# Kernel tuning notes

Measured on AMD Instinct MI355X. Metric: run time of the kernel, lower is better.

## Reference

```python
import jax, jax.numpy as jnp
import numpy as np

CH = 256
B, H, W = 8, 128, 128
CQK = CH // 8


def _conv1x1(x, w, b):
    # x: [B,C,H,W], w: [O,C], b: [O]
    return jnp.einsum('bchw,oc->bohw', x, w) + b[None, :, None, None]


def setup_inputs() -> dict:
    key = jax.random.key(0)
    ks = jax.random.split(key, 8)
    sq = 1.0 / np.sqrt(CH)
    return {
        'x': jax.random.normal(ks[0], (B, CH, H, W), dtype=jnp.float32),
        'Wq': jax.random.normal(ks[1], (CQK, CH), dtype=jnp.float32) * sq,
        'bq': jax.random.normal(ks[2], (CQK,), dtype=jnp.float32) * 0.01,
        'Wk': jax.random.normal(ks[3], (CQK, CH), dtype=jnp.float32) * sq,
        'bk': jax.random.normal(ks[4], (CQK,), dtype=jnp.float32) * 0.01,
        'Wv': jax.random.normal(ks[5], (CH, CH), dtype=jnp.float32) * sq,
        'bv': jax.random.normal(ks[6], (CH,), dtype=jnp.float32) * 0.01,
        'gamma': jax.random.normal(ks[7], (1,), dtype=jnp.float32) * 0.1,
        'recurrence': 2,
    }


def reference(x, Wq, bq, Wk, bk, Wv, bv, gamma, recurrence):
    q = _conv1x1(x, Wq, bq)   # [B, C//8, H, W]
    k = _conv1x1(x, Wk, bk)   # [B, C//8, H, W]
    v = _conv1x1(x, Wv, bv)   # [B, C, H, W]
    if recurrence % 2 == 1:
        # attention along W, independently per (b, h); no mask
        energy = jnp.einsum('bchi,bchj->bhij', q, k)      # [B,H,W,W]
        att = jax.nn.softmax(energy, axis=-1)
        out = jnp.einsum('bchj,bhij->bchi', v, att)       # [B,C,H,W]
    else:
        # attention along H, independently per (b, w); diagonal masked -inf
        energy = jnp.einsum('bciw,bcjw->bwij', q, k)      # [B,W,H,H]
        h = energy.shape[-1]
        diag = jnp.eye(h, dtype=bool)[None, None]
        energy = jnp.where(diag, -jnp.inf, energy)
        att = jax.nn.softmax(energy, axis=-1)             # [B,W,H,H]
        out = jnp.einsum('bcjw,bwij->bciw', v, att)       # [B,C,H,W]
    return gamma[0] * out + x
```

## Files before the change

### kernel.cpp

```cpp
#include <hip/hip_runtime.h>
#include <hip/hip_bf16.h>

#define B_   8
#define CH_  256
#define CQK_ 32
#define H_   128
#define W_   128

typedef __attribute__((ext_vector_type(8))) short s16x8;
typedef __attribute__((ext_vector_type(4))) float f32x4;
typedef __attribute__((ext_vector_type(4))) unsigned short u16x4;

__device__ __forceinline__ unsigned short f2b(float f) {
  __hip_bfloat16 h = __float2bfloat16(f);
  return *(unsigned short*)&h;
}
__device__ __forceinline__ float b2f(unsigned short u) {
  return __uint_as_float(((unsigned)u) << 16);
}


__global__ void kw_pack(const float* __restrict__ Wq, const float* __restrict__ Wk,
                        const float* __restrict__ Wv, unsigned short* __restrict__ wqk,
                        unsigned short* __restrict__ wv) {
  int idx = blockIdx.x * 256 + threadIdx.x;
  if (idx < 64 * 256) {
    int qc = idx >> 8, c = idx & 255;
    wqk[idx] = f2b(qc < 32 ? Wq[qc * 256 + c] : Wk[(qc - 32) * 256 + c]);
  } else {
    int i2 = idx - 64 * 256;
    wv[i2] = f2b(Wv[i2]);
  }
}

__global__ __launch_bounds__(256) void k0_xpose(const float* __restrict__ x,
                                                unsigned short* __restrict__ xt) {
  __shared__ unsigned short st[256 * 137];
  const int t = threadIdx.x;
  const int b = blockIdx.x >> 7;
  const int h = blockIdx.x & 127;
  const float* xin = x + ((size_t)b * 256 * 128 + h) * 128;
  const int w = t & 127, chalf = t >> 7;
#pragma unroll 8
  for (int it = 0; it < 128; ++it) {
    int c = it * 2 + chalf;
    st[c * 137 + w] = f2b(xin[(size_t)c * 16384 + w]);
  }
  __syncthreads();
  unsigned short* xo = xt + ((size_t)b * 128 * 128 + h) * 256;
  const int cl = t & 127, whalf = t >> 7;
#pragma unroll 8
  for (int it = 0; it < 64; ++it) {
    int wr = it * 2 + whalf;
    unsigned v = (unsigned)st[(2 * cl) * 137 + wr] |
                 ((unsigned)st[(2 * cl + 1) * 137 + wr] << 16);
    *(unsigned*)&xo[(size_t)wr * 32768 + 2 * cl] = v;
  }
}

__global__ __launch_bounds__(256, 2) void k0b_xpose(const unsigned short* __restrict__ xt,
                                                    unsigned short* __restrict__ xt2) {
  __shared__ unsigned short st[128 * 264];
  const int t = threadIdx.x;
  const size_t colbase = (size_t)blockIdx.x * 32768;
#pragma unroll
  for (int it = 0; it < 16; ++it) {
    int ch = it * 256 + t;
    int row = ch >> 5, off = (ch & 31) * 8;
    *(uint4*)&st[row * 264 + off] = *(const uint4*)&xt[colbase + ch * 8];
  }
  __syncthreads();
  const int hpl = t & 3, cq = t >> 2;
#pragma unroll 8
  for (int it = 0; it < 64; ++it) {
    const int itc = it & 3, ith = it >> 2;
    const int c = itc * 64 + cq;
    const int hp = ith * 4 + hpl;
    unsigned v = (unsigned)st[(2 * hp) * 264 + c] |
                 ((unsigned)st[(2 * hp + 1) * 264 + c] << 16);
    *(unsigned*)&xt2[colbase + (size_t)c * 128 + hp * 2] = v;
  }
}

struct SmemY {
  unsigned short qt[128 * 40];
  unsigned short kt[128 * 40];
  unsigned short att[128 * 136];
};

__global__ __launch_bounds__(256, 2)
void k1y(const unsigned short* __restrict__ xt, const unsigned short* __restrict__ xt2,
         const unsigned short* __restrict__ wqk, const float* __restrict__ bq,
         const float* __restrict__ bk, unsigned short* __restrict__ y) {
  __shared__ SmemY sm;
  const int t = threadIdx.x;
  const int wvid = t >> 6;
  const int lane = t & 63;
  const int l15 = lane & 15;
  const int quad = lane >> 4;
  const int b = blockIdx.x >> 7;
  const int w = blockIdx.x & 127;
  const size_t colbase = ((size_t)b * 128 + w) * 32768;

  {
    const int qc0 = wvid * 16;
    f32x4 acc[8];
#pragma unroll
    for (int nt = 0; nt < 8; ++nt) acc[nt] = {0.f, 0.f, 0.f, 0.f};
    const unsigned short* arow = wqk + (qc0 + l15) * 256 + quad * 8;
    const unsigned short* bcol = xt + colbase + (size_t)l15 * 256 + quad * 8;
#pragma unroll
    for (int kk = 0; kk < 8; ++kk) {
      s16x8 a = *(const s16x8*)(arow + kk * 32);
#pragma unroll
      for (int nt = 0; nt < 8; ++nt) {
        s16x8 bb = *(const s16x8*)(bcol + nt * 16 * 256 + kk * 32);
        acc[nt] = __builtin_amdgcn_mfma_f32_16x16x32_bf16(a, bb, acc[nt], 0, 0, 0);
      }
    }
    const float* bp = (wvid < 2) ? bq : bk;
    const int qcl = qc0 & 16;
    float bias[4];
#pragma unroll
    for (int r = 0; r < 4; ++r) bias[r] = bp[qcl + quad * 4 + r];
    unsigned short* dst = (wvid < 2) ? sm.qt : sm.kt;
#pragma unroll
    for (int nt = 0; nt < 8; ++nt) {
      int h = nt * 16 + l15;
      u16x4 pk;
#pragma unroll
      for (int r = 0; r < 4; ++r) pk[r] = f2b(acc[nt][r] + bias[r]);
      *(u16x4*)&dst[h * 40 + qcl + quad * 4] = pk;
    }
  }
  __syncthreads();

  {
    const int i0 = wvid * 32;
    s16x8 aQ[2];
#pragma unroll
    for (int mt = 0; mt < 2; ++mt)
      aQ[mt] = *(const s16x8*)&sm.qt[(i0 + mt * 16 + l15) * 40 + quad * 8];
    f32x4 eacc[2][8];
#pragma unroll
    for (int mt = 0; mt < 2; ++mt)
#pragma unroll
      for (int nt = 0; nt < 8; ++nt) eacc[mt][nt] = {0.f, 0.f, 0.f, 0.f};
#pragma unroll
    for (int nt = 0; nt < 8; ++nt) {
      s16x8 bK = *(const s16x8*)&sm.kt[(nt * 16 + l15) * 40 + quad * 8];
      eacc[0][nt] = __builtin_amdgcn_mfma_f32_16x16x32_bf16(aQ[0], bK, eacc[0][nt], 0, 0, 0);
      eacc[1][nt] = __builtin_amdgcn_mfma_f32_16x16x32_bf16(aQ[1], bK, eacc[1][nt], 0, 0, 0);
    }
#pragma unroll
    for (int mt = 0; mt < 2; ++mt)
#pragma unroll
      for (int nt = 0; nt < 8; ++nt) {
        const int j = nt * 16 + l15;
#pragma unroll
        for (int r = 0; r < 4; ++r)
          if (j == i0 + mt * 16 + quad * 4 + r) eacc[mt][nt][r] = -__builtin_inff();
      }
#pragma unroll
    for (int mt = 0; mt < 2; ++mt)
#pragma unroll
      for (int r = 0; r < 4; ++r) {
        float mx = -__builtin_inff();
#pragma unroll
        for (int nt = 0; nt < 8; ++nt) mx = fmaxf(mx, eacc[mt][nt][r]);
        mx = fmaxf(mx, __shfl_xor(mx, 1));
        mx = fmaxf(mx, __shfl_xor(mx, 2));
        mx = fmaxf(mx, __shfl_xor(mx, 4));
        mx = fmaxf(mx, __shfl_xor(mx, 8));
        float s = 0.f;
#pragma unroll
        for (int nt = 0; nt < 8; ++nt) {
          float p = __expf(eacc[mt][nt][r] - mx);
          eacc[mt][nt][r] = p;
          s += p;
        }
        s += __shfl_xor(s, 1);
        s += __shfl_xor(s, 2);
        s += __shfl_xor(s, 4);
        s += __shfl_xor(s, 8);
        const float inv = 1.0f / s;
        const int i = i0 + mt * 16 + quad * 4 + r;
#pragma unroll
        for (int nt = 0; nt < 8; ++nt)
          sm.att[i * 136 + nt * 16 + l15] = f2b(eacc[mt][nt][r] * inv);
      }
  }
  __syncthreads();

  f32x4 yacc[8][4];
#pragma unroll
  for (int mt = 0; mt < 8; ++mt)
#pragma unroll
    for (int nt = 0; nt < 4; ++nt) yacc[mt][nt] = {0.f, 0.f, 0.f, 0.f};
  {
    const int c0 = wvid * 64;
#pragma unroll
    for (int kj = 0; kj < 4; ++kj) {
      s16x8 aP[8];
#pragma unroll
      for (int mt = 0; mt < 8; ++mt)
        aP[mt] = *(const s16x8*)&sm.att[(mt * 16 + l15) * 136 + kj * 32 + quad * 8];
#pragma unroll
      for (int nt = 0; nt < 4; ++nt) {
        s16x8 bX = *(const s16x8*)&xt2[colbase + (size_t)(c0 + nt * 16 + l15) * 128 +
                                        kj * 32 + quad * 8];
#pragma unroll
        for (int mt = 0; mt < 8; ++mt)
          yacc[mt][nt] = __builtin_amdgcn_mfma_f32_16x16x32_bf16(aP[mt], bX, yacc[mt][nt], 0, 0, 0);
      }
    }
  }
#pragma unroll 1
  for (int h2 = 0; h2 < 2; ++h2) {
    __syncthreads();
    if ((wvid >> 1) == h2) {
      const int clb = (wvid & 1) * 64;
#pragma unroll
      for (int mt = 0; mt < 8; ++mt)
#pragma unroll
        for (int nt = 0; nt < 4; ++nt) {
          const int cl = clb + nt * 16 + l15;
#pragma unroll
          for (int r = 0; r < 4; ++r)
            sm.att[(mt * 16 + quad * 4 + r) * 136 + cl] = f2b(yacc[mt][nt][r]);
        }
    }
    __syncthreads();
#pragma unroll
    for (int it = 0; it < 8; ++it) {
      int g = it * 256 + t;
      int i = g >> 4, cc = (g & 15) * 8;
      *(uint4*)&y[((size_t)(b * 128 + i) * 128 + w) * 256 + h2 * 128 + cc] =
          *(const uint4*)&sm.att[i * 136 + cc];
    }
  }
}

__global__ __launch_bounds__(256, 2)
void k2g(const unsigned short* __restrict__ y, const unsigned short* __restrict__ wv,
         const float* __restrict__ bv, const float* __restrict__ gamma,
         const float* __restrict__ x, float* __restrict__ out) {
  const int t = threadIdx.x;
  const int wvid = t >> 6;
  const int lane = t & 63;
  const int l15 = lane & 15;
  const int quad = lane >> 4;
  const int b = blockIdx.x >> 7;
  const int h = blockIdx.x & 127;
  const int m0 = wvid * 64;
  f32x4 acc[4][8];
#pragma unroll
  for (int mt = 0; mt < 4; ++mt)
#pragma unroll
    for (int nt = 0; nt < 8; ++nt) acc[mt][nt] = {0.f, 0.f, 0.f, 0.f};
  const unsigned short* arow = wv + (m0 + l15) * 256 + quad * 8;
  const unsigned short* brow = y + ((size_t)(b * 128 + h) * 128 + l15) * 256 + quad * 8;
#pragma unroll
  for (int kk = 0; kk < 8; ++kk) {
    s16x8 a[4];
#pragma unroll
    for (int mt = 0; mt < 4; ++mt)
      a[mt] = *(const s16x8*)(arow + mt * 16 * 256 + kk * 32);
#pragma unroll
    for (int nt = 0; nt < 8; ++nt) {
      s16x8 bb = *(const s16x8*)(brow + nt * 16 * 256 + kk * 32);
#pragma unroll
      for (int mt = 0; mt < 4; ++mt)
        acc[mt][nt] = __builtin_amdgcn_mfma_f32_16x16x32_bf16(a[mt], bb, acc[mt][nt], 0, 0, 0);
    }
  }
  const float g = gamma[0];
#pragma unroll
  for (int mt = 0; mt < 4; ++mt)
#pragma unroll
    for (int r = 0; r < 4; ++r) {
      const int co = m0 + mt * 16 + quad * 4 + r;
      const float bvv = bv[co];
      const size_t base = ((size_t)(b * 256 + co) * 128 + h) * 128;
#pragma unroll
      for (int nt = 0; nt < 8; ++nt) {
        const int wc = nt * 16 + l15;
        out[base + wc] = g * (acc[mt][nt][r] + bvv) + x[base + wc];
      }
    }
}


struct SmemK1 {
  __hip_bfloat16 x[CH_][H_];
  float att[H_][130];
  union {
    struct { __hip_bfloat16 q[CQK_][H_]; __hip_bfloat16 k[CQK_][H_]; } qk;
    float vchunk[32][130];
  } s;
};

__device__ __forceinline__ void load_bf16x16(const __hip_bfloat16* p, float* f) {
  const uint4* p4 = (const uint4*)p;
  uint4 a = p4[0], b = p4[1];
  unsigned uu[8] = {a.x, a.y, a.z, a.w, b.x, b.y, b.z, b.w};
#pragma unroll
  for (int m = 0; m < 8; ++m) {
    f[2 * m] = __uint_as_float(uu[m] << 16);
    f[2 * m + 1] = __uint_as_float(uu[m] & 0xffff0000u);
  }
}

__global__ __launch_bounds__(256, 1)
void k1_attn(const float* __restrict__ x, const float* __restrict__ Wq,
             const float* __restrict__ bq, const float* __restrict__ Wk,
             const float* __restrict__ bk, const float* __restrict__ Wv,
             const float* __restrict__ bv, float* __restrict__ o_t) {
  __shared__ SmemK1 sm;
  const int t = threadIdx.x;
  const int b = blockIdx.x >> 7;
  const int w = blockIdx.x & 127;
  {
    const float* xb = x + (size_t)b * CH_ * H_ * W_ + w;
    const int h = t & 127;
    const int c0 = (t >> 7) * 128;
#pragma unroll 8
    for (int r = 0; r < 128; ++r) {
      const int c = c0 + r;
      sm.x[c][h] = __float2bfloat16(xb[(size_t)(c * H_ + h) * W_]);
    }
  }
  __syncthreads();
  {
    const int qc = t >> 3;
    const int i0 = (t & 7) << 4;
    float qa[16], ka[16];
    const float bqv = bq[qc], bkv = bk[qc];
#pragma unroll
    for (int u = 0; u < 16; ++u) { qa[u] = bqv; ka[u] = bkv; }
    const float* wqr = Wq + qc * CH_;
    const float* wkr = Wk + qc * CH_;
    for (int c = 0; c < CH_; c += 4) {
      const float4 wq4 = *(const float4*)(wqr + c);
      const float4 wk4 = *(const float4*)(wkr + c);
      const float wqs[4] = {wq4.x, wq4.y, wq4.z, wq4.w};
      const float wks[4] = {wk4.x, wk4.y, wk4.z, wk4.w};
#pragma unroll
      for (int cc = 0; cc < 4; ++cc) {
        float xf[16];
        load_bf16x16(&sm.x[c + cc][i0], xf);
#pragma unroll
        for (int u = 0; u < 16; ++u) {
          qa[u] += wqs[cc] * xf[u];
          ka[u] += wks[cc] * xf[u];
        }
      }
    }
#pragma unroll
    for (int u = 0; u < 16; ++u) {
      sm.s.qk.q[qc][i0 + u] = __float2bfloat16(qa[u]);
      sm.s.qk.k[qc][i0 + u] = __float2bfloat16(ka[u]);
    }
  }
  __syncthreads();
  {
    const int i = t >> 1;
    const int j0 = (t & 1) << 6;
    float qreg[32];
#pragma unroll
    for (int qc = 0; qc < 32; ++qc) qreg[qc] = __bfloat162float(sm.s.qk.q[qc][i]);
    float e[64];
#pragma unroll
    for (int u = 0; u < 64; ++u) e[u] = 0.0f;
    for (int qc = 0; qc < 32; ++qc) {
#pragma unroll
      for (int jc = 0; jc < 4; ++jc) {
        float kf[16];
        load_bf16x16(&sm.s.qk.k[qc][j0 + jc * 16], kf);
#pragma unroll
        for (int u = 0; u < 16; ++u) e[jc * 16 + u] += qreg[qc] * kf[u];
      }
    }
    if (i >= j0 && i < j0 + 64) e[i - j0] = -__builtin_inff();
    float m = -__builtin_inff();
#pragma unroll
    for (int u = 0; u < 64; ++u) m = fmaxf(m, e[u]);
    m = fmaxf(m, __shfl_xor(m, 1));
    float ssum = 0.0f;
#pragma unroll
    for (int u = 0; u < 64; ++u) { e[u] = __expf(e[u] - m); ssum += e[u]; }
    ssum += __shfl_xor(ssum, 1);
    const float inv = 1.0f / ssum;
#pragma unroll
    for (int u = 0; u < 64; u += 2)
      *(float2*)&sm.att[i][j0 + u] = make_float2(e[u] * inv, e[u + 1] * inv);
  }
  __syncthreads();
  const int vcc = t >> 3;
  const int vj0 = (t & 7) << 4;
  const int ai0 = (t >> 3) << 2;
  const int acc0 = (t & 7) << 2;
  for (int ch = 0; ch < 8; ++ch) {
    {
      const int cg = ch * 32 + vcc;
      float acc[16];
      const float bvv = bv[cg];
#pragma unroll
      for (int u = 0; u < 16; ++u) acc[u] = bvv;
      const float* wvr = Wv + (size_t)cg * CH_;
      for (int c = 0; c < CH_; c += 4) {
        const float4 w4 = *(const float4*)(wvr + c);
        const float ws4[4] = {w4.x, w4.y, w4.z, w4.w};
#pragma unroll
        for (int cc = 0; cc < 4; ++cc) {
          float xf[16];
          load_bf16x16(&sm.x[c + cc][vj0], xf);
#pragma unroll
          for (int u = 0; u < 16; ++u) acc[u] += ws4[cc] * xf[u];
        }
      }
#pragma unroll
      for (int m2 = 0; m2 < 8; ++m2)
        *(float2*)&sm.s.vchunk[vcc][vj0 + 2 * m2] = make_float2(acc[2 * m2], acc[2 * m2 + 1]);
    }
    __syncthreads();
    {
      float oacc[4][4];
#pragma unroll
      for (int s2 = 0; s2 < 4; ++s2)
#pragma unroll
        for (int u = 0; u < 4; ++u) oacc[s2][u] = 0.0f;
#pragma unroll 4
      for (int j = 0; j < H_; j += 2) {
        float2 av[4], vv[4];
#pragma unroll
        for (int u = 0; u < 4; ++u) av[u] = *(const float2*)&sm.att[ai0 + u][j];
#pragma unroll
        for (int s2 = 0; s2 < 4; ++s2) vv[s2] = *(const float2*)&sm.s.vchunk[acc0 + s2][j];
#pragma unroll
        for (int s2 = 0; s2 < 4; ++s2)
#pragma unroll
          for (int u = 0; u < 4; ++u)
            oacc[s2][u] += vv[s2].x * av[u].x + vv[s2].y * av[u].y;
      }
#pragma unroll
      for (int s2 = 0; s2 < 4; ++s2) {
        const int cg = ch * 32 + acc0 + s2;
        float4 st;
        st.x = oacc[s2][0]; st.y = oacc[s2][1]; st.z = oacc[s2][2]; st.w = oacc[s2][3];
        *(float4*)&o_t[(((size_t)b * CH_ + cg) * W_ + w) * H_ + ai0] = st;
      }
    }
    __syncthreads();
  }
}

__global__ __launch_bounds__(256)
void k2_epi(const float* __restrict__ o_t, const float* __restrict__ x,
            const float* __restrict__ gamma, float* __restrict__ out) {
  const int pr = blockIdx.x % 10;
  const int plane = blockIdx.x / 10;
  const int rT[10] = {0, 0, 0, 0, 1, 1, 1, 2, 2, 3};
  const int sT[10] = {0, 1, 2, 3, 1, 2, 3, 2, 3, 3};
  const int r = rT[pr], s = sT[pr];
  __shared__ float t1[32][33];
  __shared__ float t2[32][33];
  const int t = threadIdx.x;
  const size_t pbase = (size_t)plane * (H_ * W_);
  const float* ob = o_t + pbase;
#pragma unroll
  for (int ii = 0; ii < 4; ++ii) {
    const int idx = ii * 256 + t;
    const int ww = idx >> 5, hh = idx & 31;
    t1[ww][hh] = ob[(s * 32 + ww) * H_ + (r * 32 + hh)];
    if (r != s) t2[ww][hh] = ob[(r * 32 + ww) * H_ + (s * 32 + hh)];
  }
  __syncthreads();
  const float g = gamma[0];
#pragma unroll
  for (int ii = 0; ii < 4; ++ii) {
    const int idx = ii * 256 + t;
    const int hh = idx >> 5, ww = idx & 31;
    const size_t o1 = pbase + (size_t)(r * 32 + hh) * W_ + (s * 32 + ww);
    out[o1] = g * t1[ww][hh] + x[o1];
    if (r != s) {
      const size_t o2 = pbase + (size_t)(s * 32 + hh) * W_ + (r * 32 + ww);
      out[o2] = g * t2[ww][hh] + x[o2];
    }
  }
}


extern "C" void kernel_launch(void* const* d_in, const int* in_sizes, int n_in,
                              void* d_out, int out_size, void* d_ws, size_t ws_size,
                              hipStream_t stream) {
  const float* x     = (const float*)d_in[0];
  const float* Wq    = (const float*)d_in[1];
  const float* bq    = (const float*)d_in[2];
  const float* Wk    = (const float*)d_in[3];
  const float* bk    = (const float*)d_in[4];
  const float* Wv    = (const float*)d_in[5];
  const float* bv    = (const float*)d_in[6];
  const float* gamma = (const float*)d_in[7];
  float* out = (float*)d_out;

  const size_t XT   = (size_t)B_ * W_ * H_ * CH_ * 2;
  const size_t YT   = XT;
  const size_t WQKB = 64 * 256 * 2;
  const size_t WVB  = 256 * 256 * 2;
  const size_t FAST_WS = XT + YT + WQKB + WVB;

  if (ws_size >= FAST_WS) {
    unsigned short* xt  = (unsigned short*)d_ws;
    unsigned short* yb  = (unsigned short*)((char*)d_ws + XT);
    unsigned short* wqk = (unsigned short*)((char*)d_ws + XT + YT);
    unsigned short* wvb = (unsigned short*)((char*)d_ws + XT + YT + WQKB);
    unsigned short* xt2 = (unsigned short*)d_out;
    hipLaunchKernelGGL(kw_pack, dim3(320), dim3(256), 0, stream, Wq, Wk, Wv, wqk, wvb);
    hipLaunchKernelGGL(k0_xpose, dim3(B_ * H_), dim3(256), 0, stream, x, xt);
    hipLaunchKernelGGL(k0b_xpose, dim3(B_ * W_), dim3(256), 0, stream, xt, xt2);
    hipLaunchKernelGGL(k1y, dim3(B_ * W_), dim3(256), 0, stream,
                       xt, xt2, wqk, bq, bk, yb);
    hipLaunchKernelGGL(k2g, dim3(B_ * H_), dim3(256), 0, stream,
                       yb, wvb, bv, gamma, x, out);
  } else {
    const size_t OT_F = (size_t)B_ * CH_ * H_ * W_ * sizeof(float);
    float* o_t = (ws_size >= OT_F) ? (float*)d_ws : out;
    hipLaunchKernelGGL(k1_attn, dim3(B_ * W_), dim3(256), 0, stream,
                       x, Wq, bq, Wk, bk, Wv, bv, o_t);
    hipLaunchKernelGGL(k2_epi, dim3((B_ * CH_) * 10), dim3(256), 0, stream,
                       o_t, x, gamma, out);
  }
}
```

Baseline: 416.2 us.

## Fuse value projection and residual epilogue into attention kernel, stage x via LDS

Folds the former k2g kernel (Wv projection, bias, gamma scale and residual add) into k1y: the attention output y is kept in LDS and multiplied by Wv in-block, removing the global round-trip of the bf16 y buffer and one launch. The Q/K projection now stages x tiles through LDS with double-buffered global_load_lds and an XOR swizzle. Block index mapping is changed to interleave batches, and xt2 is moved from the output buffer into workspace. The trade-off is that the fused epilogue writes out with a stride of 128 floats along h (column-wise per w), so global stores and x reads become poorly coalesced, and LDS use grows.

```diff
diff --git a/kernel.cpp b/kernel.cpp
--- a/kernel.cpp
+++ b/kernel.cpp
@@ -82,24 +82,54 @@
   }
 }
 
+__device__ __forceinline__ void gld_lds16(const unsigned short* g, unsigned short* l) {
+  __builtin_amdgcn_global_load_lds(
+      (const __attribute__((address_space(1))) void*)g,
+      (__attribute__((address_space(3))) void*)l, 16, 0, 0);
+}
+
+__device__ __forceinline__ void stage_tile(const unsigned short* __restrict__ gsrc,
+                                           unsigned short* lds, int k0,
+                                           int wv_id, int lane) {
+#pragma unroll
+  for (int i = 0; i < 4; ++i) {
+    const int chunk = wv_id * 4 + i;
+    const int L = chunk * 1024 + lane * 16;
+    const int row = L >> 7;
+    const int sb = L & 127;
+    const int srcb = sb ^ ((row & 7) << 4);
+    gld_lds16(gsrc + row * 256 + k0 + (srcb >> 1), lds + chunk * 512);
+  }
+}
+
 struct SmemY {
-  unsigned short qt[128 * 40];
-  unsigned short kt[128 * 40];
-  unsigned short att[128 * 136];
+  union {
+    struct {
+      unsigned short qt[128 * 40];
+      unsigned short kt[128 * 40];
+      union {
+        unsigned short att[128 * 136];
+        unsigned short xstage[2][128 * 64];
+      } u;
+    } s;
+    unsigned short ybuf[128 * 264];
+  };
 };
 
 __global__ __launch_bounds__(256, 2)
 void k1y(const unsigned short* __restrict__ xt, const unsigned short* __restrict__ xt2,
-         const unsigned short* __restrict__ wqk, const float* __restrict__ bq,
-         const float* __restrict__ bk, unsigned short* __restrict__ y) {
+         const unsigned short* __restrict__ wqk, const unsigned short* __restrict__ wvb,
+         const float* __restrict__ bq, const float* __restrict__ bk,
+         const float* __restrict__ bv, const float* __restrict__ gamma,
+         const float* __restrict__ x, float* __restrict__ out) {
   __shared__ SmemY sm;
   const int t = threadIdx.x;
   const int wvid = t >> 6;
   const int lane = t & 63;
   const int l15 = lane & 15;
   const int quad = lane >> 4;
-  const int b = blockIdx.x >> 7;
-  const int w = blockIdx.x & 127;
+  const int b = blockIdx.x & 7;
+  const int w = blockIdx.x >> 3;
   const size_t colbase = ((size_t)b * 128 + w) * 32768;
 
   {
@@ -108,22 +138,32 @@
 #pragma unroll
     for (int nt = 0; nt < 8; ++nt) acc[nt] = {0.f, 0.f, 0.f, 0.f};
     const unsigned short* arow = wqk + (qc0 + l15) * 256 + quad * 8;
-    const unsigned short* bcol = xt + colbase + (size_t)l15 * 256 + quad * 8;
-#pragma unroll
-    for (int kk = 0; kk < 8; ++kk) {
-      s16x8 a = *(const s16x8*)(arow + kk * 32);
-#pragma unroll
-      for (int nt = 0; nt < 8; ++nt) {
-        s16x8 bb = *(const s16x8*)(bcol + nt * 16 * 256 + kk * 32);
-        acc[nt] = __builtin_amdgcn_mfma_f32_16x16x32_bf16(a, bb, acc[nt], 0, 0, 0);
-      }
+    const unsigned short* gcol = xt + colbase;
+    stage_tile(gcol, sm.s.u.xstage[0], 0, wvid, lane);
+    __syncthreads();
+#pragma unroll
+    for (int kc = 0; kc < 4; ++kc) {
+      const int cur = kc & 1;
+      if (kc < 3) stage_tile(gcol, sm.s.u.xstage[cur ^ 1], (kc + 1) * 64, wvid, lane);
+#pragma unroll
+      for (int kk2 = 0; kk2 < 2; ++kk2) {
+        s16x8 a = *(const s16x8*)(arow + (kc * 2 + kk2) * 32);
+#pragma unroll
+        for (int nt = 0; nt < 8; ++nt) {
+          const int row = nt * 16 + l15;
+          const int col = (kk2 * 64 + quad * 16) ^ ((row & 7) << 4);
+          s16x8 bb = *(const s16x8*)((const char*)sm.s.u.xstage[cur] + row * 128 + col);
+          acc[nt] = __builtin_amdgcn_mfma_f32_16x16x32_bf16(a, bb, acc[nt], 0, 0, 0);
+        }
+      }
+      __syncthreads();
     }
     const float* bp = (wvid < 2) ? bq : bk;
     const int qcl = qc0 & 16;
     float bias[4];
 #pragma unroll
     for (int r = 0; r < 4; ++r) bias[r] = bp[qcl + quad * 4 + r];
-    unsigned short* dst = (wvid < 2) ? sm.qt : sm.kt;
+    unsigned short* dst = (wvid < 2) ? sm.s.qt : sm.s.kt;
 #pragma unroll
     for (int nt = 0; nt < 8; ++nt) {
       int h = nt * 16 + l15;
@@ -140,7 +180,7 @@
     s16x8 aQ[2];
 #pragma unroll
     for (int mt = 0; mt < 2; ++mt)
-      aQ[mt] = *(const s16x8*)&sm.qt[(i0 + mt * 16 + l15) * 40 + quad * 8];
+      aQ[mt] = *(const s16x8*)&sm.s.qt[(i0 + mt * 16 + l15) * 40 + quad * 8];
     f32x4 eacc[2][8];
 #pragma unroll
     for (int mt = 0; mt < 2; ++mt)
@@ -148,7 +188,7 @@
       for (int nt = 0; nt < 8; ++nt) eacc[mt][nt] = {0.f, 0.f, 0.f, 0.f};
 #pragma unroll
     for (int nt = 0; nt < 8; ++nt) {
-      s16x8 bK = *(const s16x8*)&sm.kt[(nt * 16 + l15) * 40 + quad * 8];
+      s16x8 bK = *(const s16x8*)&sm.s.kt[(nt * 16 + l15) * 40 + quad * 8];
       eacc[0][nt] = __builtin_amdgcn_mfma_f32_16x16x32_bf16(aQ[0], bK, eacc[0][nt], 0, 0, 0);
       eacc[1][nt] = __builtin_amdgcn_mfma_f32_16x16x32_bf16(aQ[1], bK, eacc[1][nt], 0, 0, 0);
     }
@@ -187,7 +227,7 @@
         const int i = i0 + mt * 16 + quad * 4 + r;
 #pragma unroll
         for (int nt = 0; nt < 8; ++nt)
-          sm.att[i * 136 + nt * 16 + l15] = f2b(eacc[mt][nt][r] * inv);
+          sm.s.u.att[i * 136 + nt * 16 + l15] = f2b(eacc[mt][nt][r] * inv);
       }
   }
   __syncthreads();
@@ -204,7 +244,7 @@
       s16x8 aP[8];
 #pragma unroll
       for (int mt = 0; mt < 8; ++mt)
-        aP[mt] = *(const s16x8*)&sm.att[(mt * 16 + l15) * 136 + kj * 32 + quad * 8];
+        aP[mt] = *(const s16x8*)&sm.s.u.att[(mt * 16 + l15) * 136 + kj * 32 + quad * 8];
 #pragma unroll
       for (int nt = 0; nt < 4; ++nt) {
         s16x8 bX = *(const s16x8*)&xt2[colbase + (size_t)(c0 + nt * 16 + l15) * 128 +
@@ -215,79 +255,59 @@
       }
     }
   }
-#pragma unroll 1
-  for (int h2 = 0; h2 < 2; ++h2) {
-    __syncthreads();
-    if ((wvid >> 1) == h2) {
-      const int clb = (wvid & 1) * 64;
-#pragma unroll
-      for (int mt = 0; mt < 8; ++mt)
-#pragma unroll
-        for (int nt = 0; nt < 4; ++nt) {
-          const int cl = clb + nt * 16 + l15;
-#pragma unroll
-          for (int r = 0; r < 4; ++r)
-            sm.att[(mt * 16 + quad * 4 + r) * 136 + cl] = f2b(yacc[mt][nt][r]);
+  __syncthreads();
+  {
+    const int c0 = wvid * 64;
+#pragma unroll
+    for (int mt = 0; mt < 8; ++mt)
+#pragma unroll
+      for (int nt = 0; nt < 4; ++nt) {
+        const int c = c0 + nt * 16 + l15;
+#pragma unroll
+        for (int r = 0; r < 4; ++r)
+          sm.ybuf[(mt * 16 + quad * 4 + r) * 264 + c] = f2b(yacc[mt][nt][r]);
+      }
+  }
+  __syncthreads();
+
+  {
+    const int m0 = wvid * 64;
+    f32x4 oacc[4][8];
+#pragma unroll
+    for (int mt = 0; mt < 4; ++mt)
+#pragma unroll
+      for (int nt = 0; nt < 8; ++nt) oacc[mt][nt] = {0.f, 0.f, 0.f, 0.f};
+    const unsigned short* arow2 = wvb + (m0 + l15) * 256 + quad * 8;
+#pragma unroll
+    for (int kk = 0; kk < 8; ++kk) {
+      s16x8 a2[4];
+#pragma unroll
+      for (int mt = 0; mt < 4; ++mt)
+        a2[mt] = *(const s16x8*)(arow2 + mt * 16 * 256 + kk * 32);
+#pragma unroll
+      for (int nt = 0; nt < 8; ++nt) {
+        s16x8 bb = *(const s16x8*)&sm.ybuf[(nt * 16 + l15) * 264 + kk * 32 + quad * 8];
+#pragma unroll
+        for (int mt = 0; mt < 4; ++mt)
+          oacc[mt][nt] = __builtin_amdgcn_mfma_f32_16x16x32_bf16(a2[mt], bb, oacc[mt][nt], 0, 0, 0);
+      }
+    }
+    const float g = gamma[0];
+    const size_t base_bw = (size_t)b * 256 * 16384 + w;
+#pragma unroll
+    for (int mt = 0; mt < 4; ++mt)
+#pragma unroll
+      for (int r = 0; r < 4; ++r) {
+        const int co = m0 + mt * 16 + quad * 4 + r;
+        const float bvv = bv[co];
+        const size_t cbase = base_bw + (size_t)co * 16384;
+#pragma unroll
+        for (int nt = 0; nt < 8; ++nt) {
+          const int h2 = nt * 16 + l15;
+          out[cbase + h2 * 128] = g * (oacc[mt][nt][r] + bvv) + x[cbase + h2 * 128];
         }
-    }
-    __syncthreads();
-#pragma unroll
-    for (int it = 0; it < 8; ++it) {
-      int g = it * 256 + t;
-      int i = g >> 4, cc = (g & 15) * 8;
-      *(uint4*)&y[((size_t)(b * 128 + i) * 128 + w) * 256 + h2 * 128 + cc] =
-          *(const uint4*)&sm.att[i * 136 + cc];
-    }
-  }
-}
-
-__global__ __launch_bounds__(256, 2)
-void k2g(const unsigned short* __restrict__ y, const unsigned short* __restrict__ wv,
-         const float* __restrict__ bv, const float* __restrict__ gamma,
-         const float* __restrict__ x, float* __restrict__ out) {
-  const int t = threadIdx.x;
-  const int wvid = t >> 6;
-  const int lane = t & 63;
-  const int l15 = lane & 15;
-  const int quad = lane >> 4;
-  const int b = blockIdx.x >> 7;
-  const int h = blockIdx.x & 127;
-  const int m0 = wvid * 64;
-  f32x4 acc[4][8];
-#pragma unroll
-  for (int mt = 0; mt < 4; ++mt)
-#pragma unroll
-    for (int nt = 0; nt < 8; ++nt) acc[mt][nt] = {0.f, 0.f, 0.f, 0.f};
-  const unsigned short* arow = wv + (m0 + l15) * 256 + quad * 8;
-  const unsigned short* brow = y + ((size_t)(b * 128 + h) * 128 + l15) * 256 + quad * 8;
-#pragma unroll
-  for (int kk = 0; kk < 8; ++kk) {
-    s16x8 a[4];
-#pragma unroll
-    for (int mt = 0; mt < 4; ++mt)
-      a[mt] = *(const s16x8*)(arow + mt * 16 * 256 + kk * 32);
-#pragma unroll
-    for (int nt = 0; nt < 8; ++nt) {
-      s16x8 bb = *(const s16x8*)(brow + nt * 16 * 256 + kk * 32);
-#pragma unroll
-      for (int mt = 0; mt < 4; ++mt)
-        acc[mt][nt] = __builtin_amdgcn_mfma_f32_16x16x32_bf16(a[mt], bb, acc[mt][nt], 0, 0, 0);
-    }
-  }
-  const float g = gamma[0];
-#pragma unroll
-  for (int mt = 0; mt < 4; ++mt)
-#pragma unroll
-    for (int r = 0; r < 4; ++r) {
-      const int co = m0 + mt * 16 + quad * 4 + r;
-      const float bvv = bv[co];
-      const size_t base = ((size_t)(b * 256 + co) * 128 + h) * 128;
-#pragma unroll
-      for (int nt = 0; nt < 8; ++nt) {
-        const int wc = nt * 16 + l15;
-        out[base + wc] = g * (acc[mt][nt][r] + bvv) + x[base + wc];
-      }
-    }
+      }
+  }
 }
 
 
@@ -505,24 +525,21 @@
   float* out = (float*)d_out;
 
   const size_t XT   = (size_t)B_ * W_ * H_ * CH_ * 2;
-  const size_t YT   = XT;
+  const size_t XT2  = XT;
   const size_t WQKB = 64 * 256 * 2;
   const size_t WVB  = 256 * 256 * 2;
-  const size_t FAST_WS = XT + YT + WQKB + WVB;
+  const size_t FAST_WS = XT + XT2 + WQKB + WVB;
 
   if (ws_size >= FAST_WS) {
     unsigned short* xt  = (unsigned short*)d_ws;
-    unsigned short* yb  = (unsigned short*)((char*)d_ws + XT);
-    unsigned short* wqk = (unsigned short*)((char*)d_ws + XT + YT);
-    unsigned short* wvb = (unsigned short*)((char*)d_ws + XT + YT + WQKB);
-    unsigned short* xt2 = (unsigned short*)d_out;
+    unsigned short* xt2 = (unsigned short*)((char*)d_ws + XT);
+    unsigned short* wqk = (unsigned short*)((char*)d_ws + XT + XT2);
+    unsigned short* wvb = (unsigned short*)((char*)d_ws + XT + XT2 + WQKB);
     hipLaunchKernelGGL(kw_pack, dim3(320), dim3(256), 0, stream, Wq, Wk, Wv, wqk, wvb);
     hipLaunchKernelGGL(k0_xpose, dim3(B_ * H_), dim3(256), 0, stream, x, xt);
     hipLaunchKernelGGL(k0b_xpose, dim3(B_ * W_), dim3(256), 0, stream, xt, xt2);
     hipLaunchKernelGGL(k1y, dim3(B_ * W_), dim3(256), 0, stream,
-                       xt, xt2, wqk, bq, bk, yb);
-    hipLaunchKernelGGL(k2g, dim3(B_ * H_), dim3(256), 0, stream,
-                       yb, wvb, bv, gamma, x, out);
+                       xt, xt2, wqk, wvb, bq, bk, bv, gamma, x, out);
   } else {
     const size_t OT_F = (size_t)B_ * CH_ * H_ * W_ * sizeof(float);
     float* o_t = (ws_size >= OT_F) ? (float*)d_ws : out;
```

Measured after the change: 603.8 us. 1.45x slower.
